# Kernel tuning notes

Hardware: AMD Instinct MI355X
Metric: run time of the kernel (lower is better)

Reference implementation:

```python
import jax, jax.numpy as jnp
import numpy as np

N = 100_000       # nodes
E = 1_600_000     # edges
G = 128           # graphs in batch
RAW_ND, RAW_ED = 9, 3
ND, ED, H = 16, 2, 32  # node_dim, edge_dim, GAT hidden (heads=1)


def _p(key, shape, scale=0.1):
    return jax.random.normal(key, shape, dtype=jnp.float32) * scale


def setup_inputs() -> dict:
    key = jax.random.key(0)
    ks = jax.random.split(key, 32)
    inp = {
        "node_feat": jax.random.normal(ks[0], (N, RAW_ND), dtype=jnp.float32),
        "edge_index": jax.random.randint(ks[1], (2, E), 0, N, dtype=jnp.int64)
        if jax.config.jax_enable_x64 else jax.random.randint(ks[1], (2, E), 0, N).astype(jnp.int32),
        "edge_attr": jax.random.normal(ks[2], (E, RAW_ED), dtype=jnp.float32),
        "batch": jnp.sort(jax.random.randint(ks[3], (N,), 0, G)).astype(jnp.int32),
        # encoders
        "W_ne": _p(ks[4], (RAW_ND, ND)), "b_ne": jnp.zeros((ND,), jnp.float32),
        "W_ee": _p(ks[5], (RAW_ED, ED)), "b_ee": jnp.zeros((ED,), jnp.float32),
        # readout
        "W_l3": _p(ks[6], (3 * H, 1)), "b_l3": jnp.zeros((1,), jnp.float32),
    }
    dims_in = [ND, H, H]
    for i in range(3):
        k = jax.random.split(ks[7 + i], 6)
        inp[f"W{i}"] = _p(k[0], (dims_in[i], H))
        inp[f"as{i}"] = _p(k[1], (H,))
        inp[f"ad{i}"] = _p(k[2], (H,))
        inp[f"We{i}"] = _p(k[3], (ED, H))
        inp[f"ae{i}"] = _p(k[4], (H,))
        inp[f"bb{i}"] = jnp.zeros((H,), jnp.float32)
    return inp


def _segment_softmax(logits, seg, num_segments):
    m = jax.ops.segment_max(logits, seg, num_segments=num_segments)
    m = jnp.where(jnp.isfinite(m), m, 0.0)
    e = jnp.exp(logits - m[seg])
    s = jax.ops.segment_sum(e, seg, num_segments=num_segments)
    return e / (s[seg] + 1e-16)


def _gat(x, src, dst, ef, W, a_s, a_d, We, a_e, b):
    # PyG GATConv, heads=1, negative_slope=0.2
    h = x @ W                                   # [N', H]
    a_src = h @ a_s                             # [N']
    a_dst = h @ a_d
    a_edge = (ef @ We) @ a_e                    # [E']
    logits = jax.nn.leaky_relu(a_src[src] + a_dst[dst] + a_edge, 0.2)
    att = _segment_softmax(logits, dst, h.shape[0])
    out = jax.ops.segment_sum(h[src] * att[:, None], dst, num_segments=h.shape[0])
    return out + b


def reference(node_feat, edge_index, edge_attr, batch,
              W_ne, b_ne, W_ee, b_ee, W_l3, b_l3,
              W0, as0, ad0, We0, ae0, bb0,
              W1, as1, ad1, We1, ae1, bb1,
              W2, as2, ad2, We2, ae2, bb2):
    n = node_feat.shape[0]
    x = node_feat @ W_ne + b_ne                 # NodeEncoder -> [N,16]
    ef = edge_attr @ W_ee + b_ee                # EdgeEncoder -> [E,2]
    # add_self_loops=True with fill_value='mean' (PyG default when edge_dim set)
    loop = jnp.arange(n, dtype=edge_index.dtype)
    src = jnp.concatenate([edge_index[0], loop])
    dst = jnp.concatenate([edge_index[1], loop])
    ef_fill = jnp.broadcast_to(ef.mean(axis=0), (n, ef.shape[1]))
    ef_aug = jnp.concatenate([ef, ef_fill], axis=0)
    x1 = _gat(x, src, dst, ef_aug, W0, as0, ad0, We0, ae0, bb0)
    x2 = _gat(x1, src, dst, ef_aug, W1, as1, ad1, We1, ae1, bb1)
    x3 = _gat(x2, src, dst, ef_aug, W2, as2, ad2, We2, ae2, bb2)
    x_cat = jnp.concatenate([x1, x2, x3], axis=1)  # [N, 96]
    sums = jax.ops.segment_sum(x_cat, batch, num_segments=G)
    cnt = jax.ops.segment_sum(jnp.ones((n,), x_cat.dtype), batch, num_segments=G)
    pooled = sums / jnp.maximum(cnt, 1.0)[:, None]   # global mean pool [G,96]
    return pooled @ W_l3 + b_l3                      # [G,1]
```

## Files before the change

kernel.cpp:

```cpp
#include <hip/hip_runtime.h>
#include <hip/hip_fp16.h>


#define NBUCK_SHIFT 8
#define NBUCK_MAX 512
#define CAP 6144

__global__ void k_pre(const float* __restrict__ nf, const float* __restrict__ Wne,
                      const float* __restrict__ bne, float* __restrict__ x0,
                      const float4* __restrict__ ea4, const float* __restrict__ Wee,
                      const float* __restrict__ bee, float2* __restrict__ partial,
                      const int* __restrict__ ei1, int* __restrict__ bucket_cnt,
                      const int* __restrict__ batch, int* __restrict__ bounds,
                      int n, int e, int ep, int nbNE, int nbCS, int nbH) {
    int b = blockIdx.x, t = threadIdx.x;
    if (b < nbNE) {
        int gid = b * 256 + t;
        if (gid >= n * 16) return;
        int node = gid >> 4, j = gid & 15;
        const float* xr = nf + node * 9;
        float acc = bne[j];
#pragma unroll
        for (int k = 0; k < 9; ++k) acc += xr[k] * Wne[k * 16 + j];
        x0[gid] = acc;
        return;
    }
    b -= nbNE;
    if (b < nbCS) {
        int tid = b * 256 + t;
        int e4 = e >> 2;
        float s0 = 0.f, s1 = 0.f;
        if (tid < e4) {
            float4 q0 = ea4[tid * 3], q1 = ea4[tid * 3 + 1], q2 = ea4[tid * 3 + 2];
            float a = q0.x + q0.w + q1.z + q2.y;
            float b2 = q0.y + q1.x + q1.w + q2.z;
            float c = q0.z + q1.y + q2.x + q2.w;
            s0 = a * Wee[0] + b2 * Wee[2] + c * Wee[4] + 4.f * bee[0];
            s1 = a * Wee[1] + b2 * Wee[3] + c * Wee[5] + 4.f * bee[1];
        }
#pragma unroll
        for (int off = 32; off > 0; off >>= 1) {
            s0 += __shfl_xor(s0, off, 64);
            s1 += __shfl_xor(s1, off, 64);
        }
        if ((t & 63) == 0)
            partial[(b << 2) + (t >> 6)] = make_float2(s0, s1);
        return;
    }
    b -= nbCS;
    if (b < nbH) {
        __shared__ int lh[NBUCK_MAX];
        lh[t] = 0; lh[t + 256] = 0;
        __syncthreads();
        int base = b * 4096;
#pragma unroll
        for (int i = 0; i < 16; ++i) {
            int gid = base + i * 256 + t;
            if (gid < ep) {
                int d = (gid < e) ? ei1[gid] : gid - e;
                atomicAdd(&lh[d >> NBUCK_SHIFT], 1);
            }
        }
        __syncthreads();
        if (lh[t]) atomicAdd(&bucket_cnt[t], lh[t]);
        if (lh[t + 256]) atomicAdd(&bucket_cnt[t + 256], lh[t + 256]);
        return;
    }
    for (int g = t; g <= 128; g += 256) {
        if (g == 128) { bounds[128] = n; continue; }
        int lo = 0, hi = n;
        while (lo < hi) {
            int mid = (lo + hi) >> 1;
            if (batch[mid] < g) lo = mid + 1; else hi = mid;
        }
        bounds[g] = lo;
    }
}

__global__ void __launch_bounds__(512)
k_mid(const float* __restrict__ We0, const float* __restrict__ ae0,
      const float* __restrict__ We1, const float* __restrict__ ae1,
      const float* __restrict__ We2, const float* __restrict__ ae2,
      const float2* __restrict__ partial, int nw, float einv,
      float* __restrict__ consts,
      const int* __restrict__ bucket_cnt, int* __restrict__ bucket_base,
      int* __restrict__ bcursor, int nbuck, int ep, int* __restrict__ rp, int n) {
    int t = threadIdx.x;
    if (blockIdx.x == 0) {
        __shared__ float r0[512], r1[512];
        float m0 = 0.f, m1 = 0.f;
        for (int i = t; i < nw; i += 512) {
            float2 v = partial[i];
            m0 += v.x; m1 += v.y;
        }
        r0[t] = m0; r1[t] = m1;
        __syncthreads();
        for (int o = 256; o > 0; o >>= 1) {
            if (t < o) { r0[t] += r0[t + o]; r1[t] += r1[t + o]; }
            __syncthreads();
        }
        if (t == 0) {
            consts[12] = r0[0] * einv;
            consts[13] = r1[0] * einv;
            const float* We[3] = {We0, We1, We2};
            const float* ae[3] = {ae0, ae1, ae2};
            for (int l = 0; l < 3; ++l) {
                float c0 = 0.f, c1 = 0.f;
                for (int j = 0; j < 32; ++j) {
                    c0 += We[l][j] * ae[l][j];
                    c1 += We[l][32 + j] * ae[l][j];
                }
                consts[l * 2 + 0] = c0;
                consts[l * 2 + 1] = c1;
            }
        }
    } else {
        __shared__ int s[512];
        int v = (t < nbuck) ? bucket_cnt[t] : 0;
        s[t] = v;
        __syncthreads();
        for (int o = 1; o < 512; o <<= 1) {
            int x = (t >= o) ? s[t - o] : 0;
            __syncthreads();
            s[t] += x;
            __syncthreads();
        }
        int ex = s[t] - v;
        if (t < nbuck) { bucket_base[t] = ex; bcursor[t] = ex; }
        if (t == 0) { bucket_base[nbuck] = ep; rp[n] = ep; }
    }
}

__global__ void k_binB(const int* __restrict__ ei0, const int* __restrict__ ei1,
                       const float* __restrict__ ea, const float* __restrict__ We,
                       const float* __restrict__ be, const float* __restrict__ consts,
                       int* __restrict__ bcursor, uint2* __restrict__ st, int e, int ep) {
    __shared__ int lh[NBUCK_MAX], lcur[NBUCK_MAX];
    int t = threadIdx.x;
    lh[t] = 0; lh[t + 256] = 0;
    __syncthreads();
    int base = blockIdx.x * 4096;
    unsigned int sd[16], fh[16];
    int bk[16];
    float w00 = We[0], w10 = We[2], w20 = We[4];
    float w01 = We[1], w11 = We[3], w21 = We[5];
    float b0 = be[0], b1 = be[1];
#pragma unroll
    for (int i = 0; i < 16; ++i) {
        int gid = base + i * 256 + t;
        bk[i] = -1;
        if (gid < ep) {
            int s, d; float f0, f1;
            if (gid < e) {
                s = ei0[gid]; d = ei1[gid];
                const float* r = ea + (size_t)gid * 3;
                float a0 = r[0], a1 = r[1], a2 = r[2];
                f0 = a0 * w00 + a1 * w10 + a2 * w20 + b0;
                f1 = a0 * w01 + a1 * w11 + a2 * w21 + b1;
            } else {
                s = d = gid - e;
                f0 = consts[12]; f1 = consts[13];
            }
            bk[i] = d >> NBUCK_SHIFT;
            sd[i] = ((unsigned int)s << NBUCK_SHIFT) | (unsigned int)(d & 255);
            __half2 hh = __floats2half2_rn(f0, f1);
            fh[i] = *reinterpret_cast<unsigned int*>(&hh);
            atomicAdd(&lh[bk[i]], 1);
        }
    }
    __syncthreads();
    if (lh[t] > 0) lcur[t] = atomicAdd(&bcursor[t], lh[t]);
    if (lh[t + 256] > 0) lcur[t + 256] = atomicAdd(&bcursor[t + 256], lh[t + 256]);
    __syncthreads();
#pragma unroll
    for (int i = 0; i < 16; ++i) {
        if (bk[i] >= 0) {
            int pos = atomicAdd(&lcur[bk[i]], 1);
            st[pos] = make_uint2(sd[i], fh[i]);
        }
    }
}

__global__ void __launch_bounds__(512)
k_binC(const uint2* __restrict__ st, const int* __restrict__ bucket_base,
       int* __restrict__ rp, uint2* __restrict__ rec, int n) {
    __shared__ int nh[256], ns[256];
    __shared__ uint2 rs[CAP];
    int k = blockIdx.x, t = threadIdx.x;
    int s0 = bucket_base[k], s1 = bucket_base[k + 1];
    int cnt = s1 - s0;
    if (t < 256) nh[t] = 0;
    __syncthreads();
    for (int i = s0 + t; i < s1; i += 512)
        atomicAdd(&nh[st[i].x & 255], 1);
    __syncthreads();
    if (t < 256) ns[t] = nh[t];
    __syncthreads();
    for (int o = 1; o < 256; o <<= 1) {
        int add = 0;
        if (t < 256 && t >= o) add = ns[t - o];
        __syncthreads();
        if (t < 256) ns[t] += add;
        __syncthreads();
    }
    int node0 = k << NBUCK_SHIFT;
    if (t < 256) {
        int startl = ns[t] - nh[t];
        if (node0 + t < n) rp[node0 + t] = s0 + startl;
        nh[t] = startl;
    }
    __syncthreads();
    for (int i = s0 + t; i < s1; i += 512) {
        uint2 v = st[i];
        int pos = atomicAdd(&nh[v.x & 255], 1);
        uint2 r = make_uint2(v.x >> NBUCK_SHIFT, v.y);
        if (pos < CAP) rs[pos] = r;
        else rec[s0 + pos] = r;
    }
    __syncthreads();
    int m = cnt < CAP ? cnt : CAP;
    for (int i = t; i < m; i += 512)
        rec[s0 + i] = rs[i];
}

template <int K>
__global__ void k_hproj(const float* __restrict__ x, const float* __restrict__ W,
                        const float* __restrict__ as_, const float* __restrict__ ad_,
                        unsigned int* __restrict__ h2, float* __restrict__ asrc,
                        float* __restrict__ adst, int n) {
    __shared__ float sW[K * 32];
    for (int i = threadIdx.x; i < K * 32; i += 256) sW[i] = W[i];
    __syncthreads();
    int node = blockIdx.x * 8 + (threadIdx.x >> 5);
    int j = threadIdx.x & 31;
    if (node >= n) return;
    const float* xr = x + (size_t)node * K;
    float acc = 0.f;
#pragma unroll
    for (int k = 0; k < K; ++k) acc += xr[k] * sW[k * 32 + j];
    float accp = __shfl_down(acc, 1, 32);
    if ((j & 1) == 0) {
        __half2 hh = __floats2half2_rn(acc, accp);
        h2[(size_t)node * 16 + (j >> 1)] = *reinterpret_cast<unsigned int*>(&hh);
    }
    float r1 = acc * as_[j], r2 = acc * ad_[j];
    for (int off = 16; off > 0; off >>= 1) {
        r1 += __shfl_xor(r1, off, 32);
        r2 += __shfl_xor(r2, off, 32);
    }
    if (j == 0) { asrc[node] = r1; adst[node] = r2; }
}

__device__ __forceinline__ float h2_get(const unsigned int* __restrict__ h2,
                                        int s, int word, bool hi) {
    unsigned int hw = h2[(size_t)s * 16 + word];
    __half2 hh = *reinterpret_cast<__half2*>(&hw);
    return hi ? __high2float(hh) : __low2float(hh);
}

__global__ void k_agg(const int* __restrict__ rp, const uint2* __restrict__ rec,
                      const float* __restrict__ asrc, const float* __restrict__ adst,
                      const float* __restrict__ consts, const unsigned int* __restrict__ h2,
                      const float* __restrict__ bb, float* __restrict__ xout,
                      int n, int layer) {
    int node = blockIdx.x * 8 + (threadIdx.x >> 5);
    int j = threadIdx.x & 31;
    if (node >= n) return;
    float c0 = consts[layer * 2], c1 = consts[layer * 2 + 1];
    int r0 = rp[node], r1 = rp[node + 1];
    float adn = adst[node];
    int word = j >> 1;
    bool hi = (j & 1) != 0;
    float acc = 0.f, psum = 0.f;
    for (int c = r0; c < r1; c += 32) {
        int i = c + j;
        float pe = 0.f; int s = 0;
        if (i < r1) {
            unsigned long long rv = __builtin_nontemporal_load(
                reinterpret_cast<const unsigned long long*>(rec + i));
            s = (int)(unsigned int)(rv & 0xffffffffull);
            unsigned int fv = (unsigned int)(rv >> 32);
            __half2 hh = *reinterpret_cast<__half2*>(&fv);
            float lg = asrc[s] + adn + __low2float(hh) * c0 + __high2float(hh) * c1;
            lg = lg > 0.f ? lg : 0.2f * lg;
            pe = __expf(lg);
        }
        psum += pe;
        int cnt = min(32, r1 - c);
        int t = 0;
        for (; t + 8 <= cnt; t += 8) {
            int s0 = __shfl(s, t, 32),     s1 = __shfl(s, t + 1, 32);
            int s2 = __shfl(s, t + 2, 32), s3 = __shfl(s, t + 3, 32);
            int s4 = __shfl(s, t + 4, 32), s5 = __shfl(s, t + 5, 32);
            int s6 = __shfl(s, t + 6, 32), s7 = __shfl(s, t + 7, 32);
            float p0 = __shfl(pe, t, 32),     p1 = __shfl(pe, t + 1, 32);
            float p2 = __shfl(pe, t + 2, 32), p3 = __shfl(pe, t + 3, 32);
            float p4 = __shfl(pe, t + 4, 32), p5 = __shfl(pe, t + 5, 32);
            float p6 = __shfl(pe, t + 6, 32), p7 = __shfl(pe, t + 7, 32);
            float h0 = h2_get(h2, s0, word, hi);
            float h1 = h2_get(h2, s1, word, hi);
            float h2v = h2_get(h2, s2, word, hi);
            float h3 = h2_get(h2, s3, word, hi);
            float h4 = h2_get(h2, s4, word, hi);
            float h5 = h2_get(h2, s5, word, hi);
            float h6 = h2_get(h2, s6, word, hi);
            float h7 = h2_get(h2, s7, word, hi);
            acc += p0 * h0; acc += p1 * h1; acc += p2 * h2v; acc += p3 * h3;
            acc += p4 * h4; acc += p5 * h5; acc += p6 * h6; acc += p7 * h7;
        }
        for (; t + 4 <= cnt; t += 4) {
            int s0 = __shfl(s, t, 32),     s1 = __shfl(s, t + 1, 32);
            int s2 = __shfl(s, t + 2, 32), s3 = __shfl(s, t + 3, 32);
            float p0 = __shfl(pe, t, 32),     p1 = __shfl(pe, t + 1, 32);
            float p2 = __shfl(pe, t + 2, 32), p3 = __shfl(pe, t + 3, 32);
            float h0 = h2_get(h2, s0, word, hi);
            float h1 = h2_get(h2, s1, word, hi);
            float h2v = h2_get(h2, s2, word, hi);
            float h3 = h2_get(h2, s3, word, hi);
            acc += p0 * h0; acc += p1 * h1; acc += p2 * h2v; acc += p3 * h3;
        }
        for (; t < cnt; ++t) {
            int st2 = __shfl(s, t, 32);
            float pt = __shfl(pe, t, 32);
            acc += pt * h2_get(h2, st2, word, hi);
        }
    }
#pragma unroll
    for (int off = 16; off > 0; off >>= 1) psum += __shfl_xor(psum, off, 32);
    xout[(size_t)node * 32 + j] = acc / (psum + 1e-16f) + bb[j];
}

__global__ void k_dot3(const float2* __restrict__ x1, const float2* __restrict__ x2,
                       const float2* __restrict__ x3, const int* __restrict__ bounds,
                       const float* __restrict__ Wl3, const float* __restrict__ bl3,
                       float* __restrict__ out) {
    __shared__ float red[256];
    int g = blockIdx.x, t = threadIdx.x;
    int s0 = bounds[g], s1 = bounds[g + 1];
    int cnt = s1 - s0;
    int w = t & 15;
    const float2* W2 = reinterpret_cast<const float2*>(Wl3);
    float2 w1 = W2[w], w2 = W2[16 + w], w3 = W2[32 + w];
    float v = 0.f;
    for (int i = t; i < cnt * 16; i += 256) {
        int node = s0 + (i >> 4);
        float2 a1 = x1[(size_t)node * 16 + w];
        float2 a2 = x2[(size_t)node * 16 + w];
        float2 a3 = x3[(size_t)node * 16 + w];
        v += a1.x * w1.x + a1.y * w1.y
           + a2.x * w2.x + a2.y * w2.y
           + a3.x * w3.x + a3.y * w3.y;
    }
    red[t] = v;
    __syncthreads();
    for (int o = 128; o > 0; o >>= 1) {
        if (t < o) red[t] += red[t + o];
        __syncthreads();
    }
    if (t == 0) {
        float c = (float)cnt;
        if (c < 1.f) c = 1.f;
        out[g] = red[0] / c + bl3[0];
    }
}

extern "C" void kernel_launch(void* const* d_in, const int* in_sizes, int n_in,
                              void* d_out, int out_size, void* d_ws, size_t ws_size,
                              hipStream_t stream) {
    (void)n_in; (void)out_size; (void)ws_size;
    const float* nf    = (const float*)d_in[0];
    const int*   ei    = (const int*)d_in[1];
    const float* ea    = (const float*)d_in[2];
    const int*   batch = (const int*)d_in[3];
    const float* W_ne  = (const float*)d_in[4];
    const float* b_ne  = (const float*)d_in[5];
    const float* W_ee  = (const float*)d_in[6];
    const float* b_ee  = (const float*)d_in[7];
    const float* W_l3  = (const float*)d_in[8];
    const float* b_l3  = (const float*)d_in[9];
    const float *Wl[3], *asl[3], *adl[3], *Wel[3], *ael[3], *bbl[3];
    for (int l = 0; l < 3; ++l) {
        Wl[l]  = (const float*)d_in[10 + 6 * l];
        asl[l] = (const float*)d_in[11 + 6 * l];
        adl[l] = (const float*)d_in[12 + 6 * l];
        Wel[l] = (const float*)d_in[13 + 6 * l];
        ael[l] = (const float*)d_in[14 + 6 * l];
        bbl[l] = (const float*)d_in[15 + 6 * l];
    }

    const int n  = in_sizes[3];
    const int e  = in_sizes[2] / 3;
    const int ep = e + n;
    const int* ei0 = ei;
    const int* ei1 = ei + e;
    const int nbuck = (n + 255) >> NBUCK_SHIFT;

    char* w = (char*)d_ws;
    size_t off = 0;
    auto alloc = [&](size_t b) { size_t o = off; off = (off + b + 255) & ~(size_t)255; return o; };
    float*        x0      = (float*)(w + alloc((size_t)n * 16 * 4));
    float*        x1      = (float*)(w + alloc((size_t)n * 32 * 4));
    float*        x2      = (float*)(w + alloc((size_t)n * 32 * 4));
    float*        x3      = (float*)(w + alloc((size_t)n * 32 * 4));
    unsigned int* h2      = (unsigned int*)(w + alloc((size_t)n * 16 * 4));
    float*        asrc    = (float*)(w + alloc((size_t)n * 4));
    float*        adst    = (float*)(w + alloc((size_t)n * 4));
    uint2*        st      = (uint2*)(w + alloc((size_t)ep * 8));
    uint2*        rec     = (uint2*)(w + alloc((size_t)ep * 8));
    int*          rp      = (int*)(w + alloc((size_t)(n + 1) * 4));
    int*          bcnt    = (int*)(w + alloc(NBUCK_MAX * 4));
    int*          bbase   = (int*)(w + alloc((NBUCK_MAX + 1) * 4));
    int*          bcur    = (int*)(w + alloc(NBUCK_MAX * 4));
    float2*       partial = (float2*)(w + alloc((size_t)8192 * 8));
    float*        consts  = (float*)(w + alloc(256));
    int*          bounds  = (int*)(w + alloc(129 * 4));

    hipMemsetAsync(bcnt, 0, NBUCK_MAX * 4, stream);

    int e4   = e >> 2;
    int nbNE = (n * 16 + 255) / 256;
    int nbCS = (e4 + 255) / 256;
    int nbH  = (ep + 4095) / 4096;
    int nw   = nbCS * 4;

    k_pre<<<nbNE + nbCS + nbH + 1, 256, 0, stream>>>(
        nf, W_ne, b_ne, x0, (const float4*)ea, W_ee, b_ee, partial,
        ei1, bcnt, batch, bounds, n, e, ep, nbNE, nbCS, nbH);
    k_mid<<<2, 512, 0, stream>>>(Wel[0], ael[0], Wel[1], ael[1], Wel[2], ael[2],
                                 partial, nw, 1.0f / (float)e, consts,
                                 bcnt, bbase, bcur, nbuck, ep, rp, n);
    k_binB<<<nbH, 256, 0, stream>>>(ei0, ei1, ea, W_ee, b_ee, consts, bcur, st, e, ep);
    k_binC<<<nbuck, 512, 0, stream>>>(st, bbase, rp, rec, n);

    const float* xin = x0;
    float* xo[3] = {x1, x2, x3};
    for (int l = 0; l < 3; ++l) {
        if (l == 0)
            k_hproj<16><<<(n + 7) / 8, 256, 0, stream>>>(xin, Wl[l], asl[l], adl[l],
                                                         h2, asrc, adst, n);
        else
            k_hproj<32><<<(n + 7) / 8, 256, 0, stream>>>(xin, Wl[l], asl[l], adl[l],
                                                         h2, asrc, adst, n);
        k_agg<<<(n + 7) / 8, 256, 0, stream>>>(rp, rec, asrc, adst, consts,
                                               h2, bbl[l], xo[l], n, l);
        xin = xo[l];
    }
    k_dot3<<<128, 256, 0, stream>>>((const float2*)x1, (const float2*)x2,
                                    (const float2*)x3, bounds, W_l3, b_l3,
                                    (float*)d_out);
}
```

Measured before the change: 382.3 us.

## Fuse next-layer projection and readout dot into aggregation kernels

```diff
diff --git a/kernel.cpp b/kernel.cpp
--- a/kernel.cpp
+++ b/kernel.cpp
@@ -6,26 +6,14 @@
 #define NBUCK_MAX 512
 #define CAP 6144
 
-__global__ void k_pre(const float* __restrict__ nf, const float* __restrict__ Wne,
-                      const float* __restrict__ bne, float* __restrict__ x0,
-                      const float4* __restrict__ ea4, const float* __restrict__ Wee,
+__global__ void k_pre(const float4* __restrict__ ea4, const float* __restrict__ Wee,
                       const float* __restrict__ bee, float2* __restrict__ partial,
                       const int* __restrict__ ei1, int* __restrict__ bucket_cnt,
                       const int* __restrict__ batch, int* __restrict__ bounds,
-                      int n, int e, int ep, int nbNE, int nbCS, int nbH) {
+                      const float* __restrict__ Wne, const float* __restrict__ bne,
+                      const float* __restrict__ W0, float* __restrict__ wf,
+                      int n, int e, int ep, int nbCS, int nbH) {
     int b = blockIdx.x, t = threadIdx.x;
-    if (b < nbNE) {
-        int gid = b * 256 + t;
-        if (gid >= n * 16) return;
-        int node = gid >> 4, j = gid & 15;
-        const float* xr = nf + node * 9;
-        float acc = bne[j];
-#pragma unroll
-        for (int k = 0; k < 9; ++k) acc += xr[k] * Wne[k * 16 + j];
-        x0[gid] = acc;
-        return;
-    }
-    b -= nbNE;
     if (b < nbCS) {
         int tid = b * 256 + t;
         int e4 = e >> 2;
@@ -66,6 +54,17 @@
         if (lh[t + 256]) atomicAdd(&bucket_cnt[t + 256], lh[t + 256]);
         return;
     }
+    for (int i = t; i < 288; i += 256) {
+        int m = i >> 5, j = i & 31;
+        float a = 0.f;
+        for (int k = 0; k < 16; ++k) a += Wne[m * 16 + k] * W0[k * 32 + j];
+        wf[i] = a;
+    }
+    if (t < 32) {
+        float a = 0.f;
+        for (int k = 0; k < 16; ++k) a += bne[k] * W0[k * 32 + t];
+        wf[288 + t] = a;
+    }
     for (int g = t; g <= 128; g += 256) {
         if (g == 128) { bounds[128] = n; continue; }
         int lo = 0, hi = n;
@@ -75,6 +74,31 @@
         }
         bounds[g] = lo;
     }
+}
+
+__global__ void k_hproj0(const float* __restrict__ nf, const float* __restrict__ wf,
+                         const float* __restrict__ as_, const float* __restrict__ ad_,
+                         unsigned int* __restrict__ h2, float* __restrict__ asrc,
+                         float* __restrict__ adst, int n) {
+    int node = blockIdx.x * 8 + (threadIdx.x >> 5);
+    int j = threadIdx.x & 31;
+    if (node >= n) return;
+    const float* xr = nf + node * 9;
+    float acc = wf[288 + j];
+#pragma unroll
+    for (int m = 0; m < 9; ++m) acc += xr[m] * wf[m * 32 + j];
+    float accp = __shfl_down(acc, 1, 32);
+    if ((j & 1) == 0) {
+        __half2 hh = __floats2half2_rn(acc, accp);
+        h2[(size_t)node * 16 + (j >> 1)] = *reinterpret_cast<unsigned int*>(&hh);
+    }
+    float r1 = acc * as_[j], r2 = acc * ad_[j];
+#pragma unroll
+    for (int off = 16; off > 0; off >>= 1) {
+        r1 += __shfl_xor(r1, off, 32);
+        r2 += __shfl_xor(r2, off, 32);
+    }
+    if (j == 0) { asrc[node] = r1; adst[node] = r2; }
 }
 
 __global__ void __launch_bounds__(512)
@@ -223,34 +247,6 @@
         rec[s0 + i] = rs[i];
 }
 
-template <int K>
-__global__ void k_hproj(const float* __restrict__ x, const float* __restrict__ W,
-                        const float* __restrict__ as_, const float* __restrict__ ad_,
-                        unsigned int* __restrict__ h2, float* __restrict__ asrc,
-                        float* __restrict__ adst, int n) {
-    __shared__ float sW[K * 32];
-    for (int i = threadIdx.x; i < K * 32; i += 256) sW[i] = W[i];
-    __syncthreads();
-    int node = blockIdx.x * 8 + (threadIdx.x >> 5);
-    int j = threadIdx.x & 31;
-    if (node >= n) return;
-    const float* xr = x + (size_t)node * K;
-    float acc = 0.f;
-#pragma unroll
-    for (int k = 0; k < K; ++k) acc += xr[k] * sW[k * 32 + j];
-    float accp = __shfl_down(acc, 1, 32);
-    if ((j & 1) == 0) {
-        __half2 hh = __floats2half2_rn(acc, accp);
-        h2[(size_t)node * 16 + (j >> 1)] = *reinterpret_cast<unsigned int*>(&hh);
-    }
-    float r1 = acc * as_[j], r2 = acc * ad_[j];
-    for (int off = 16; off > 0; off >>= 1) {
-        r1 += __shfl_xor(r1, off, 32);
-        r2 += __shfl_xor(r2, off, 32);
-    }
-    if (j == 0) { asrc[node] = r1; adst[node] = r2; }
-}
-
 __device__ __forceinline__ float h2_get(const unsigned int* __restrict__ h2,
                                         int s, int word, bool hi) {
     unsigned int hw = h2[(size_t)s * 16 + word];
@@ -258,17 +254,26 @@
     return hi ? __high2float(hh) : __low2float(hh);
 }
 
+template <bool HAS_NEXT>
 __global__ void k_agg(const int* __restrict__ rp, const uint2* __restrict__ rec,
-                      const float* __restrict__ asrc, const float* __restrict__ adst,
-                      const float* __restrict__ consts, const unsigned int* __restrict__ h2,
-                      const float* __restrict__ bb, float* __restrict__ xout,
-                      int n, int layer) {
+                      const float* __restrict__ asrcIn, const float* __restrict__ adstIn,
+                      const float* __restrict__ consts, const unsigned int* __restrict__ h2in,
+                      const float* __restrict__ bb, const float* __restrict__ Wn,
+                      const float* __restrict__ asn, const float* __restrict__ adn_,
+                      unsigned int* __restrict__ h2out, float* __restrict__ asrcOut,
+                      float* __restrict__ adstOut, const float* __restrict__ wl3,
+                      float* __restrict__ vout, int n, int layer) {
+    __shared__ float sW[1024];
+    if (HAS_NEXT) {
+        for (int i = threadIdx.x; i < 1024; i += 256) sW[i] = Wn[i];
+        __syncthreads();
+    }
     int node = blockIdx.x * 8 + (threadIdx.x >> 5);
     int j = threadIdx.x & 31;
     if (node >= n) return;
     float c0 = consts[layer * 2], c1 = consts[layer * 2 + 1];
     int r0 = rp[node], r1 = rp[node + 1];
-    float adn = adst[node];
+    float adn = adstIn[node];
     int word = j >> 1;
     bool hi = (j & 1) != 0;
     float acc = 0.f, psum = 0.f;
@@ -281,7 +286,7 @@
             s = (int)(unsigned int)(rv & 0xffffffffull);
             unsigned int fv = (unsigned int)(rv >> 32);
             __half2 hh = *reinterpret_cast<__half2*>(&fv);
-            float lg = asrc[s] + adn + __low2float(hh) * c0 + __high2float(hh) * c1;
+            float lg = asrcIn[s] + adn + __low2float(hh) * c0 + __high2float(hh) * c1;
             lg = lg > 0.f ? lg : 0.2f * lg;
             pe = __expf(lg);
         }
@@ -297,14 +302,14 @@
             float p2 = __shfl(pe, t + 2, 32), p3 = __shfl(pe, t + 3, 32);
             float p4 = __shfl(pe, t + 4, 32), p5 = __shfl(pe, t + 5, 32);
             float p6 = __shfl(pe, t + 6, 32), p7 = __shfl(pe, t + 7, 32);
-            float h0 = h2_get(h2, s0, word, hi);
-            float h1 = h2_get(h2, s1, word, hi);
-            float h2v = h2_get(h2, s2, word, hi);
-            float h3 = h2_get(h2, s3, word, hi);
-            float h4 = h2_get(h2, s4, word, hi);
-            float h5 = h2_get(h2, s5, word, hi);
-            float h6 = h2_get(h2, s6, word, hi);
-            float h7 = h2_get(h2, s7, word, hi);
+            float h0 = h2_get(h2in, s0, word, hi);
+            float h1 = h2_get(h2in, s1, word, hi);
+            float h2v = h2_get(h2in, s2, word, hi);
+            float h3 = h2_get(h2in, s3, word, hi);
+            float h4 = h2_get(h2in, s4, word, hi);
+            float h5 = h2_get(h2in, s5, word, hi);
+            float h6 = h2_get(h2in, s6, word, hi);
+            float h7 = h2_get(h2in, s7, word, hi);
             acc += p0 * h0; acc += p1 * h1; acc += p2 * h2v; acc += p3 * h3;
             acc += p4 * h4; acc += p5 * h5; acc += p6 * h6; acc += p7 * h7;
         }
@@ -313,52 +318,61 @@
             int s2 = __shfl(s, t + 2, 32), s3 = __shfl(s, t + 3, 32);
             float p0 = __shfl(pe, t, 32),     p1 = __shfl(pe, t + 1, 32);
             float p2 = __shfl(pe, t + 2, 32), p3 = __shfl(pe, t + 3, 32);
-            float h0 = h2_get(h2, s0, word, hi);
-            float h1 = h2_get(h2, s1, word, hi);
-            float h2v = h2_get(h2, s2, word, hi);
-            float h3 = h2_get(h2, s3, word, hi);
+            float h0 = h2_get(h2in, s0, word, hi);
+            float h1 = h2_get(h2in, s1, word, hi);
+            float h2v = h2_get(h2in, s2, word, hi);
+            float h3 = h2_get(h2in, s3, word, hi);
             acc += p0 * h0; acc += p1 * h1; acc += p2 * h2v; acc += p3 * h3;
         }
         for (; t < cnt; ++t) {
             int st2 = __shfl(s, t, 32);
             float pt = __shfl(pe, t, 32);
-            acc += pt * h2_get(h2, st2, word, hi);
+            acc += pt * h2_get(h2in, st2, word, hi);
         }
     }
 #pragma unroll
     for (int off = 16; off > 0; off >>= 1) psum += __shfl_xor(psum, off, 32);
-    xout[(size_t)node * 32 + j] = acc / (psum + 1e-16f) + bb[j];
-}
-
-__global__ void k_dot3(const float2* __restrict__ x1, const float2* __restrict__ x2,
-                       const float2* __restrict__ x3, const int* __restrict__ bounds,
-                       const float* __restrict__ Wl3, const float* __restrict__ bl3,
-                       float* __restrict__ out) {
+    float res = acc / (psum + 1e-16f) + bb[j];
+    float v = res * wl3[j];
+#pragma unroll
+    for (int off = 16; off > 0; off >>= 1) v += __shfl_xor(v, off, 32);
+    if (j == 0) vout[node] = v;
+    if (HAS_NEXT) {
+        float hn = 0.f;
+#pragma unroll
+        for (int k = 0; k < 32; ++k)
+            hn += __shfl(res, k, 32) * sW[k * 32 + j];
+        float hnp = __shfl_down(hn, 1, 32);
+        if ((j & 1) == 0) {
+            __half2 hh = __floats2half2_rn(hn, hnp);
+            h2out[(size_t)node * 16 + (j >> 1)] = *reinterpret_cast<unsigned int*>(&hh);
+        }
+        float r1n = hn * asn[j], r2n = hn * adn_[j];
+#pragma unroll
+        for (int off = 16; off > 0; off >>= 1) {
+            r1n += __shfl_xor(r1n, off, 32);
+            r2n += __shfl_xor(r2n, off, 32);
+        }
+        if (j == 0) { asrcOut[node] = r1n; adstOut[node] = r2n; }
+    }
+}
+
+__global__ void k_dotv(const float* __restrict__ v0, const float* __restrict__ v1,
+                       const float* __restrict__ v2, const int* __restrict__ bounds,
+                       const float* __restrict__ bl3, float* __restrict__ out) {
     __shared__ float red[256];
     int g = blockIdx.x, t = threadIdx.x;
     int s0 = bounds[g], s1 = bounds[g + 1];
-    int cnt = s1 - s0;
-    int w = t & 15;
-    const float2* W2 = reinterpret_cast<const float2*>(Wl3);
-    float2 w1 = W2[w], w2 = W2[16 + w], w3 = W2[32 + w];
-    float v = 0.f;
-    for (int i = t; i < cnt * 16; i += 256) {
-        int node = s0 + (i >> 4);
-        float2 a1 = x1[(size_t)node * 16 + w];
-        float2 a2 = x2[(size_t)node * 16 + w];
-        float2 a3 = x3[(size_t)node * 16 + w];
-        v += a1.x * w1.x + a1.y * w1.y
-           + a2.x * w2.x + a2.y * w2.y
-           + a3.x * w3.x + a3.y * w3.y;
-    }
-    red[t] = v;
+    float acc = 0.f;
+    for (int i = s0 + t; i < s1; i += 256) acc += v0[i] + v1[i] + v2[i];
+    red[t] = acc;
     __syncthreads();
     for (int o = 128; o > 0; o >>= 1) {
         if (t < o) red[t] += red[t + o];
         __syncthreads();
     }
     if (t == 0) {
-        float c = (float)cnt;
+        float c = (float)(s1 - s0);
         if (c < 1.f) c = 1.f;
         out[g] = red[0] / c + bl3[0];
     }
@@ -398,13 +412,15 @@
     char* w = (char*)d_ws;
     size_t off = 0;
     auto alloc = [&](size_t b) { size_t o = off; off = (off + b + 255) & ~(size_t)255; return o; };
-    float*        x0      = (float*)(w + alloc((size_t)n * 16 * 4));
-    float*        x1      = (float*)(w + alloc((size_t)n * 32 * 4));
-    float*        x2      = (float*)(w + alloc((size_t)n * 32 * 4));
-    float*        x3      = (float*)(w + alloc((size_t)n * 32 * 4));
-    unsigned int* h2      = (unsigned int*)(w + alloc((size_t)n * 16 * 4));
-    float*        asrc    = (float*)(w + alloc((size_t)n * 4));
-    float*        adst    = (float*)(w + alloc((size_t)n * 4));
+    unsigned int* h2a     = (unsigned int*)(w + alloc((size_t)n * 16 * 4));
+    unsigned int* h2b     = (unsigned int*)(w + alloc((size_t)n * 16 * 4));
+    float*        asrcA   = (float*)(w + alloc((size_t)n * 4));
+    float*        adstA   = (float*)(w + alloc((size_t)n * 4));
+    float*        asrcB   = (float*)(w + alloc((size_t)n * 4));
+    float*        adstB   = (float*)(w + alloc((size_t)n * 4));
+    float*        v0      = (float*)(w + alloc((size_t)n * 4));
+    float*        v1      = (float*)(w + alloc((size_t)n * 4));
+    float*        v2      = (float*)(w + alloc((size_t)n * 4));
     uint2*        st      = (uint2*)(w + alloc((size_t)ep * 8));
     uint2*        rec     = (uint2*)(w + alloc((size_t)ep * 8));
     int*          rp      = (int*)(w + alloc((size_t)(n + 1) * 4));
@@ -414,38 +430,36 @@
     float2*       partial = (float2*)(w + alloc((size_t)8192 * 8));
     float*        consts  = (float*)(w + alloc(256));
     int*          bounds  = (int*)(w + alloc(129 * 4));
+    float*        wfbuf   = (float*)(w + alloc(320 * 4));
 
     hipMemsetAsync(bcnt, 0, NBUCK_MAX * 4, stream);
 
     int e4   = e >> 2;
-    int nbNE = (n * 16 + 255) / 256;
     int nbCS = (e4 + 255) / 256;
     int nbH  = (ep + 4095) / 4096;
     int nw   = nbCS * 4;
-
-    k_pre<<<nbNE + nbCS + nbH + 1, 256, 0, stream>>>(
-        nf, W_ne, b_ne, x0, (const float4*)ea, W_ee, b_ee, partial,
-        ei1, bcnt, batch, bounds, n, e, ep, nbNE, nbCS, nbH);
+    int nbN  = (n + 7) / 8;
+
+    k_pre<<<nbCS + nbH + 1, 256, 0, stream>>>(
+        (const float4*)ea, W_ee, b_ee, partial, ei1, bcnt, batch, bounds,
+        W_ne, b_ne, Wl[0], wfbuf, n, e, ep, nbCS, nbH);
+    k_hproj0<<<nbN, 256, 0, stream>>>(nf, wfbuf, asl[0], adl[0],
+                                      h2a, asrcA, adstA, n);
     k_mid<<<2, 512, 0, stream>>>(Wel[0], ael[0], Wel[1], ael[1], Wel[2], ael[2],
                                  partial, nw, 1.0f / (float)e, consts,
                                  bcnt, bbase, bcur, nbuck, ep, rp, n);
     k_binB<<<nbH, 256, 0, stream>>>(ei0, ei1, ea, W_ee, b_ee, consts, bcur, st, e, ep);
     k_binC<<<nbuck, 512, 0, stream>>>(st, bbase, rp, rec, n);
 
-    const float* xin = x0;
-    float* xo[3] = {x1, x2, x3};
-    for (int l = 0; l < 3; ++l) {
-        if (l == 0)
-            k_hproj<16><<<(n + 7) / 8, 256, 0, stream>>>(xin, Wl[l], asl[l], adl[l],
-                                                         h2, asrc, adst, n);
-        else
-            k_hproj<32><<<(n + 7) / 8, 256, 0, stream>>>(xin, Wl[l], asl[l], adl[l],
-                                                         h2, asrc, adst, n);
-        k_agg<<<(n + 7) / 8, 256, 0, stream>>>(rp, rec, asrc, adst, consts,
-                                               h2, bbl[l], xo[l], n, l);
-        xin = xo[l];
-    }
-    k_dot3<<<128, 256, 0, stream>>>((const float2*)x1, (const float2*)x2,
-                                    (const float2*)x3, bounds, W_l3, b_l3,
-                                    (float*)d_out);
-}
+    k_agg<true><<<nbN, 256, 0, stream>>>(rp, rec, asrcA, adstA, consts, h2a,
+                                         bbl[0], Wl[1], asl[1], adl[1],
+                                         h2b, asrcB, adstB, W_l3 + 0, v0, n, 0);
+    k_agg<true><<<nbN, 256, 0, stream>>>(rp, rec, asrcB, adstB, consts, h2b,
+                                         bbl[1], Wl[2], asl[2], adl[2],
+                                         h2a, asrcA, adstA, W_l3 + 32, v1, n, 1);
+    k_agg<false><<<nbN, 256, 0, stream>>>(rp, rec, asrcA, adstA, consts, h2a,
+                                          bbl[2], nullptr, nullptr, nullptr,
+                                          nullptr, nullptr, nullptr,
+                                          W_l3 + 64, v2, n, 2);
+    k_dotv<<<128, 256, 0, stream>>>(v0, v1, v2, bounds, b_l3, (float*)d_out);
+}
```

Measured after the change: 362.0 us. 1.06x faster.
